# Optimization experiments

Measured on AMD Instinct MI355X. Metric: run time of the kernel, lower is better.

The kernel has to match this reference:

```python
import jax, jax.numpy as jnp
import numpy as np
from jax import lax

DIM = 128
T = 16
KSIZE = 7


def make_decay_mask(kernel_size, decay_rate=0.3):
    center = kernel_size // 2
    y, x = jnp.meshgrid(jnp.arange(kernel_size), jnp.arange(kernel_size))
    dist = jnp.sqrt((x - center) ** 2 + (y - center) ** 2)
    return jnp.exp(-decay_rate * dist / center)


def kernel_to_freq(kernel, H, W):
    # Scatter k x k kernel to wrapped positions of an H x W grid, then FFT.
    C, k, _ = kernel.shape
    center = k // 2
    target_i = (jnp.arange(k) - center) % H
    target_j = (jnp.arange(k) - center) % W
    ti, tj = jnp.meshgrid(target_i, target_j, indexing='ij')
    padded = jnp.zeros((C, H, W), dtype=kernel.dtype).at[:, ti, tj].set(kernel)
    return jnp.fft.fft2(padded, axes=(-2, -1))  # (C, H, W) complex


def complex_to_realimag_chw(x_f):
    # complex (C,H,W) -> real (1,H,W,2C)
    x_ri = jnp.concatenate([x_f.real, x_f.imag], axis=0)
    return x_ri.transpose(1, 2, 0)[None, ...]


def setup_inputs() -> dict:
    key = jax.random.key(0)
    k1, k2, k3 = jax.random.split(key, 3)
    x_ri = jax.random.normal(k1, (8, 128, 128, 2 * DIM), dtype=jnp.float32)
    A = 0.02 * jax.random.normal(k2, (DIM, KSIZE, KSIZE), dtype=jnp.float32)
    B = 0.02 * jax.random.normal(k3, (DIM, KSIZE, KSIZE), dtype=jnp.float32)
    return {"x_ri": x_ri, "A": A, "B": B}


def reference(x_ri, A, B):
    Bt, H, W, C2 = x_ri.shape
    C = C2 // 2
    decay = make_decay_mask(KSIZE, decay_rate=0.3)
    A_spatial = 0.9 * jnp.tanh(A * decay[None, :, :])
    A_f_ri = complex_to_realimag_chw(kernel_to_freq(A_spatial, H, W)).astype(x_ri.dtype)
    B_f_ri = complex_to_realimag_chw(kernel_to_freq(B, H, W)).astype(x_ri.dtype)

    A_r, A_i = A_f_ri[..., :C], A_f_ri[..., C:]
    B_r, B_i = B_f_ri[..., :C], B_f_ri[..., C:]
    x_r, x_i = x_ri[..., :C], x_ri[..., C:]
    # Bx is constant across scan steps
    Bx_r = B_r * x_r - B_i * x_i
    Bx_i = B_r * x_i + B_i * x_r

    def step_fn(h_ri, _):
        h_r, h_i = h_ri[..., :C], h_ri[..., C:]
        h_new_r = A_r * h_r - A_i * h_i + Bx_r
        h_new_i = A_r * h_i + A_i * h_r + Bx_i
        return jnp.concatenate([h_new_r, h_new_i], axis=-1), None

    h_init = jnp.zeros_like(x_ri)
    h_final, _ = lax.scan(step_fn, h_init, None, length=T)
    return h_final
```

## Files before the change

### kernel.cpp

```cpp
#include <hip/hip_runtime.h>
#include <math.h>

#define NCH   128
#define HH    128
#define WW    128
#define NB    8
#define KS    7
#define MSIZE (128*7*128)

__device__ float g_MAr[MSIZE];
__device__ float g_MAi[MSIZE];
__device__ float g_MBr[MSIZE];
__device__ float g_MBi[MSIZE];

__global__ void kern_factor(const float* __restrict__ A, const float* __restrict__ B) {
    int idx = blockIdx.x * blockDim.x + threadIdx.x;
    if (idx >= MSIZE) return;
    int c  = idx & 127;
    int ub = idx >> 7;
    int b  = ub % 7;
    int u  = ub / 7;

    const float W0 = -6.283185307179586f / 128.0f;
    float mar = 0.f, mai = 0.f, mbr = 0.f, mbi = 0.f;
    float db = (float)(b - 3);
#pragma unroll
    for (int a = 0; a < 7; ++a) {
        float da   = (float)(a - 3);
        float dist = sqrtf(da * da + db * db);
        float dec  = expf(-0.1f * dist);
        float ka   = 0.9f * tanhf(A[c * 49 + a * 7 + b] * dec);
        float kb   = B[c * 49 + a * 7 + b];
        float th   = W0 * (float)(u * (a - 3));
        float s, cc;
        sincosf(th, &s, &cc);
        mar = fmaf(ka, cc, mar);
        mai = fmaf(ka, s,  mai);
        mbr = fmaf(kb, cc, mbr);
        mbi = fmaf(kb, s,  mbi);
    }
    g_MAr[idx] = mar;
    g_MAi[idx] = mai;
    g_MBr[idx] = mbr;
    g_MBi[idx] = mbi;
}

__global__ void kern_main(const float* __restrict__ x, float* __restrict__ out) {
    __shared__ float s_cs[128];
    __shared__ float s_sn[128];
    int t = threadIdx.x;
    if (t < 128) {
        float th = (6.283185307179586f / 128.0f) * (float)t;
        float s, c;
        sincosf(th, &s, &c);
        s_cs[t] = c;
        s_sn[t] = s;
    }
    __syncthreads();

    int bid = blockIdx.x;
    int u   = bid >> 4;
    int v   = ((bid & 15) << 3) + (t >> 5);
    int c0  = (t & 31) << 2;

    float Afr[4] = {0, 0, 0, 0}, Afi[4] = {0, 0, 0, 0};
    float Bfr[4] = {0, 0, 0, 0}, Bfi[4] = {0, 0, 0, 0};

#pragma unroll
    for (int b = 0; b < 7; ++b) {
        int p = (v * (b - 3)) & 127;
        float wr = s_cs[p];
        float wi = -s_sn[p];
        int mbase = (u * 7 + b) * 128 + c0;
        float mar[4], mai[4], mbr[4], mbi[4];
        *(float4*)mar = *(const float4*)(g_MAr + mbase);
        *(float4*)mai = *(const float4*)(g_MAi + mbase);
        *(float4*)mbr = *(const float4*)(g_MBr + mbase);
        *(float4*)mbi = *(const float4*)(g_MBi + mbase);
#pragma unroll
        for (int j = 0; j < 4; ++j) {
            Afr[j] = fmaf(mar[j], wr, fmaf(-mai[j], wi, Afr[j]));
            Afi[j] = fmaf(mar[j], wi, fmaf( mai[j], wr, Afi[j]));
            Bfr[j] = fmaf(mbr[j], wr, fmaf(-mbi[j], wi, Bfr[j]));
            Bfi[j] = fmaf(mbr[j], wi, fmaf( mbi[j], wr, Bfi[j]));
        }
    }

    float cr[4], ci[4];
#pragma unroll
    for (int j = 0; j < 4; ++j) {
        float ar = Afr[j], ai = Afi[j];
        float a2r = ar * ar - ai * ai,   a2i = 2.f * ar * ai;
        float a4r = a2r * a2r - a2i * a2i, a4i = 2.f * a2r * a2i;
        float a8r = a4r * a4r - a4i * a4i, a8i = 2.f * a4r * a4i;
        float s1r = 1.f + ar,  s1i = ai;
        float s2r = 1.f + a2r, s2i = a2i;
        float pr  = s1r * s2r - s1i * s2i;
        float pi  = s1r * s2i + s1i * s2r;
        float s3r = 1.f + a4r, s3i = a4i;
        float qr  = pr * s3r - pi * s3i;
        float qi  = pr * s3i + pi * s3r;
        float s4r = 1.f + a8r, s4i = a8i;
        float Sr  = qr * s4r - qi * s4i;
        float Si  = qr * s4i + qi * s4r;
        cr[j] = Sr * Bfr[j] - Si * Bfi[j];
        ci[j] = Sr * Bfi[j] + Si * Bfr[j];
    }

#pragma unroll
    for (int bt = 0; bt < NB; ++bt) {
        size_t base = (((size_t)bt * HH + u) * WW + v) * (2 * NCH) + c0;
        float xr[4], xi[4], orr[4], oii[4];
        *(float4*)xr = *(const float4*)(x + base);
        *(float4*)xi = *(const float4*)(x + base + NCH);
#pragma unroll
        for (int j = 0; j < 4; ++j) {
            orr[j] = cr[j] * xr[j] - ci[j] * xi[j];
            oii[j] = cr[j] * xi[j] + ci[j] * xr[j];
        }
        *(float4*)(out + base)       = *(const float4*)orr;
        *(float4*)(out + base + NCH) = *(const float4*)oii;
    }
}

extern "C" void kernel_launch(void* const* d_in, const int* in_sizes, int n_in,
                              void* d_out, int out_size, void* d_ws, size_t ws_size,
                              hipStream_t stream) {
    const float* x = (const float*)d_in[0];
    const float* A = (const float*)d_in[1];
    const float* B = (const float*)d_in[2];
    float* out = (float*)d_out;

    kern_factor<<<(MSIZE + 255) / 256, 256, 0, stream>>>(A, B);
    kern_main<<<2048, 256, 0, stream>>>(x, out);
}
```

Baseline: 60.34 us.

## Split coefficient computation from streaming pass and use nontemporal output stores

Moves computation of the per-(u,v,c) transfer coefficient into its own kernel, which writes it to a 16 MB global buffer. A separate streaming kernel then reads the coefficients and applies them to the batch with nontemporal stores. The aim is to keep the memory-bound streaming pass free of the coefficient work and to avoid polluting the cache with output. The cost is an extra kernel launch and an extra 16 MB write plus read of coefficients.

```diff
diff --git a/kernel.cpp b/kernel.cpp
--- a/kernel.cpp
+++ b/kernel.cpp
@@ -7,11 +7,16 @@
 #define NB    8
 #define KS    7
 #define MSIZE (128*7*128)
+#define CSIZE (128*128*128)
+
+typedef float f32x4 __attribute__((ext_vector_type(4)));
 
 __device__ float g_MAr[MSIZE];
 __device__ float g_MAi[MSIZE];
 __device__ float g_MBr[MSIZE];
 __device__ float g_MBi[MSIZE];
+__device__ float g_Cr[CSIZE];
+__device__ float g_Ci[CSIZE];
 
 __global__ void kern_factor(const float* __restrict__ A, const float* __restrict__ B) {
     int idx = blockIdx.x * blockDim.x + threadIdx.x;
@@ -45,7 +50,7 @@
     g_MBi[idx] = mbi;
 }
 
-__global__ void kern_main(const float* __restrict__ x, float* __restrict__ out) {
+__global__ void kern_coef() {
     __shared__ float s_cs[128];
     __shared__ float s_sn[128];
     int t = threadIdx.x;
@@ -72,11 +77,10 @@
         float wr = s_cs[p];
         float wi = -s_sn[p];
         int mbase = (u * 7 + b) * 128 + c0;
-        float mar[4], mai[4], mbr[4], mbi[4];
-        *(float4*)mar = *(const float4*)(g_MAr + mbase);
-        *(float4*)mai = *(const float4*)(g_MAi + mbase);
-        *(float4*)mbr = *(const float4*)(g_MBr + mbase);
-        *(float4*)mbi = *(const float4*)(g_MBi + mbase);
+        f32x4 mar = *(const f32x4*)(g_MAr + mbase);
+        f32x4 mai = *(const f32x4*)(g_MAi + mbase);
+        f32x4 mbr = *(const f32x4*)(g_MBr + mbase);
+        f32x4 mbi = *(const f32x4*)(g_MBi + mbase);
 #pragma unroll
         for (int j = 0; j < 4; ++j) {
             Afr[j] = fmaf(mar[j], wr, fmaf(-mai[j], wi, Afr[j]));
@@ -86,11 +90,11 @@
         }
     }
 
-    float cr[4], ci[4];
+    f32x4 cr, ci;
 #pragma unroll
     for (int j = 0; j < 4; ++j) {
         float ar = Afr[j], ai = Afi[j];
-        float a2r = ar * ar - ai * ai,   a2i = 2.f * ar * ai;
+        float a2r = ar * ar - ai * ai,     a2i = 2.f * ar * ai;
         float a4r = a2r * a2r - a2i * a2i, a4i = 2.f * a2r * a2i;
         float a8r = a4r * a4r - a4i * a4i, a8i = 2.f * a4r * a4i;
         float s1r = 1.f + ar,  s1i = ai;
@@ -107,19 +111,35 @@
         ci[j] = Sr * Bfi[j] + Si * Bfr[j];
     }
 
+    int cbase = ((u << 7) | v) * 128 + c0;
+    *(f32x4*)(g_Cr + cbase) = cr;
+    *(f32x4*)(g_Ci + cbase) = ci;
+}
+
+__global__ void kern_stream(const float* __restrict__ x, float* __restrict__ out) {
+    int t   = threadIdx.x;
+    int bid = blockIdx.x;
+    int u   = bid >> 4;
+    int v   = ((bid & 15) << 3) + (t >> 5);
+    int c0  = (t & 31) << 2;
+
+    int cbase = ((u << 7) | v) * 128 + c0;
+    f32x4 cr = *(const f32x4*)(g_Cr + cbase);
+    f32x4 ci = *(const f32x4*)(g_Ci + cbase);
+
 #pragma unroll
     for (int bt = 0; bt < NB; ++bt) {
         size_t base = (((size_t)bt * HH + u) * WW + v) * (2 * NCH) + c0;
-        float xr[4], xi[4], orr[4], oii[4];
-        *(float4*)xr = *(const float4*)(x + base);
-        *(float4*)xi = *(const float4*)(x + base + NCH);
+        f32x4 xr = *(const f32x4*)(x + base);
+        f32x4 xi = *(const f32x4*)(x + base + NCH);
+        f32x4 orr, oii;
 #pragma unroll
         for (int j = 0; j < 4; ++j) {
             orr[j] = cr[j] * xr[j] - ci[j] * xi[j];
             oii[j] = cr[j] * xi[j] + ci[j] * xr[j];
         }
-        *(float4*)(out + base)       = *(const float4*)orr;
-        *(float4*)(out + base + NCH) = *(const float4*)oii;
+        __builtin_nontemporal_store(orr, (f32x4*)(out + base));
+        __builtin_nontemporal_store(oii, (f32x4*)(out + base + NCH));
     }
 }
 
@@ -132,5 +152,6 @@
     float* out = (float*)d_out;
 
     kern_factor<<<(MSIZE + 255) / 256, 256, 0, stream>>>(A, B);
-    kern_main<<<2048, 256, 0, stream>>>(x, out);
+    kern_coef<<<2048, 256, 0, stream>>>();
+    kern_stream<<<2048, 256, 0, stream>>>(x, out);
 }
```

Measured after the change: 64.10 us. +6.2%, slower.
